# Kernel optimization log

Hardware: AMD Instinct MI355X
Metric: run time of the kernel (lower is better)

## Reference

```python
import jax, jax.numpy as jnp
import numpy as np

N = 40000
E = 640000
D_IN = 128
HID = 128


def _sage_conv(x_src, x_dst, edge_index, W_l, b_l, W_r):
    """PyG SAGEConv with mean aggregation.
    out = lin_l(mean_{j in N(i)} x_src[j]) + lin_r(x_dst[i])
    (lin_l carries the bias; lin_r has bias=False in PyG.)
    """
    src, dst = edge_index[0], edge_index[1]
    n = x_dst.shape[0]
    # gather neighbor (source) features, scatter-sum to targets
    msg_sum = jax.ops.segment_sum(x_src[src], dst, num_segments=n)  # [N, d]
    deg = jax.ops.segment_sum(jnp.ones((src.shape[0],), x_src.dtype), dst,
                              num_segments=n)  # [N]
    agg = msg_sum / jnp.maximum(deg, 1.0)[:, None]  # mean over in-neighbors
    return agg @ W_l + b_l + x_dst @ W_r


def setup_inputs() -> dict:
    key = jax.random.key(0)
    ks = jax.random.split(key, 8)
    s_in = 1.0 / np.sqrt(D_IN)
    s_h = 1.0 / np.sqrt(HID)
    return {
        "x": jax.random.normal(ks[0], (N, D_IN), jnp.float32),
        "edge_index": jax.random.randint(ks[1], (2, E), 0, N, jnp.int64)
                      if jax.config.jax_enable_x64 else
                      jax.random.randint(ks[1], (2, E), 0, N, jnp.int32),
        "W1_l": jax.random.normal(ks[2], (D_IN, HID), jnp.float32) * s_in,
        "b1": jax.random.normal(ks[3], (HID,), jnp.float32) * s_in,
        "W1_r": jax.random.normal(ks[4], (D_IN, HID), jnp.float32) * s_in,
        "W2_l": jax.random.normal(ks[5], (HID, HID), jnp.float32) * s_h,
        "b2": jax.random.normal(ks[6], (HID,), jnp.float32) * s_h,
        "W2_r": jax.random.normal(ks[7], (HID, HID), jnp.float32) * s_h,
    }


def reference(x, edge_index, W1_l, b1, W1_r, W2_l, b2, W2_r):
    h = _sage_conv(x, x, edge_index, W1_l, b1, W1_r)
    h = jax.nn.relu(h)
    out = _sage_conv(h, h, edge_index, W2_l, b2, W2_r)
    return out
```

## Files before the change

### kernel.cpp

```cpp
#include <hip/hip_runtime.h>
#include <hip/hip_bf16.h>

#define NN 40000
#define NE 640000
#define DD 128
#define SLOT 128

typedef unsigned short u16;
typedef unsigned int u32;
typedef __attribute__((ext_vector_type(8))) short short8v;
typedef __attribute__((ext_vector_type(4))) float f32x4;

__device__ __forceinline__ u16 f2b(float f) {
  __hip_bfloat16 h = __float2bfloat16(f);
  return *reinterpret_cast<u16*>(&h);
}

#define TOB_N (NN * DD / 4)
#define WCVT_N 65536
__global__ void setup_kernel(const float* __restrict__ x,
                             const float* __restrict__ W1l, const float* __restrict__ W1r,
                             const float* __restrict__ W2l, const float* __restrict__ W2r,
                             u16* __restrict__ xb, u16* __restrict__ wt1,
                             u16* __restrict__ wt2, int* __restrict__ cnt,
                             u16* __restrict__ hb) {
  int i = blockIdx.x * 256 + threadIdx.x;
  if (i < TOB_N) {
    float4 v = *(const float4*)(x + (size_t)i * 4);
    ushort4 o;
    o.x = f2b(v.x); o.y = f2b(v.y); o.z = f2b(v.z); o.w = f2b(v.w);
    *(ushort4*)(xb + (size_t)i * 4) = o;
  } else if (i < TOB_N + WCVT_N) {
    int j = i - TOB_N;
    int layer = j >> 15;
    int jj = j & 32767;
    int n = jj >> 8, k = jj & 255;
    const float* W = layer ? ((k < 128) ? W2l : W2r) : ((k < 128) ? W1l : W1r);
    u16* Wt = layer ? wt2 : wt1;
    Wt[jj] = f2b(W[(size_t)(k & 127) * 128 + n]);
  } else if (i < TOB_N + WCVT_N + NN) {
    cnt[i - TOB_N - WCVT_N] = 0;
  } else if (i < TOB_N + WCVT_N + NN + 128) {
    int j = i - TOB_N - WCVT_N - NN;
    u32* p = (j < 64) ? ((u32*)(xb + (size_t)NN * DD) + j)
                      : ((u32*)(hb + (size_t)NN * DD) + (j - 64));
    *p = 0u;
  }
}

__global__ void fill2_kernel(const int* __restrict__ src, const int* __restrict__ dst,
                             int* __restrict__ cnt, int* __restrict__ csr) {
  int e = blockIdx.x * 256 + threadIdx.x;
  if (e < NE) {
    int d = dst[e];
    int p = atomicAdd(&cnt[d], 1);
    if (p < SLOT) __builtin_nontemporal_store(src[e], &csr[(size_t)d * SLOT + p]);
  }
}

template <int OUT_BF16, int RELU>
__global__ __launch_bounds__(256) void fused_kernel(
    const u16* __restrict__ feat, const int* __restrict__ cnt,
    const int* __restrict__ csr, const u16* __restrict__ Wt,
    const float* __restrict__ bias, void* __restrict__ outp) {
  __shared__ u16 As[2][16][128];
  const int t = threadIdx.x;
  const int w = t >> 6;
  const int lane = t & 63;
  const int li = lane & 15;
  const int eo = lane >> 4;
  const int tile = blockIdx.x * 16;
  const int node0 = tile + w * 4;

  {
    const int j = w * 4 + eo;
    const uint4 s = *(const uint4*)(feat + (size_t)(tile + j) * DD + li * 8);
    *(uint4*)((char*)&As[1][j][0] + ((li * 16) ^ ((j & 7) << 4))) = s;
  }

  int n[4];
  float inv[4];
#pragma unroll
  for (int s = 0; s < 4; ++s) {
    const int d = cnt[node0 + s];
    n[s] = (d < SLOT) ? d : SLOT;
    inv[s] = 1.0f / (float)(d > 1 ? d : 1);
  }
  int nmax = max(max(n[0], n[1]), max(n[2], n[3]));

  float acc[4][8];
#pragma unroll
  for (int s = 0; s < 4; ++s)
#pragma unroll
    for (int j = 0; j < 8; ++j) acc[s][j] = 0.f;

  const int* crow0 = csr + (size_t)node0 * SLOT;
  for (int it = eo; it < nmax; it += 4) {
    int srcn[4];
#pragma unroll
    for (int s = 0; s < 4; ++s)
      srcn[s] = (it < n[s]) ? crow0[s * SLOT + it] : NN;
    uint4 v[4];
#pragma unroll
    for (int s = 0; s < 4; ++s)
      v[s] = *(const uint4*)(feat + (size_t)srcn[s] * DD + li * 8);
#pragma unroll
    for (int s = 0; s < 4; ++s) {
      acc[s][0] += __uint_as_float(v[s].x << 16);
      acc[s][1] += __uint_as_float(v[s].x & 0xffff0000u);
      acc[s][2] += __uint_as_float(v[s].y << 16);
      acc[s][3] += __uint_as_float(v[s].y & 0xffff0000u);
      acc[s][4] += __uint_as_float(v[s].z << 16);
      acc[s][5] += __uint_as_float(v[s].z & 0xffff0000u);
      acc[s][6] += __uint_as_float(v[s].w << 16);
      acc[s][7] += __uint_as_float(v[s].w & 0xffff0000u);
    }
  }
#pragma unroll
  for (int s = 0; s < 4; ++s)
#pragma unroll
    for (int j = 0; j < 8; ++j) {
      acc[s][j] += __shfl_xor(acc[s][j], 16, 64);
      acc[s][j] += __shfl_xor(acc[s][j], 32, 64);
    }
  if (eo == 0) {
#pragma unroll
    for (int s = 0; s < 4; ++s) {
      u16 r8[8];
#pragma unroll
      for (int j = 0; j < 8; ++j) r8[j] = f2b(acc[s][j] * inv[s]);
      uint4 o;
      o.x = (u32)r8[0] | ((u32)r8[1] << 16);
      o.y = (u32)r8[2] | ((u32)r8[3] << 16);
      o.z = (u32)r8[4] | ((u32)r8[5] << 16);
      o.w = (u32)r8[6] | ((u32)r8[7] << 16);
      const int j = w * 4 + s;
      *(uint4*)((char*)&As[0][j][0] + ((li * 16) ^ ((j & 7) << 4))) = o;
    }
  }
  __syncthreads();

  const int r = li;
  const int g = eo;
  f32x4 acc2[2];
  acc2[0] = (f32x4){0.f, 0.f, 0.f, 0.f};
  acc2[1] = (f32x4){0.f, 0.f, 0.f, 0.f};
#pragma unroll
  for (int ks = 0; ks < 8; ++ks) {
    const int sel = ks >> 2;
    const int c0 = (ks & 3) * 32 + g * 8;
    const short8v afr =
        *(const short8v*)((const char*)&As[sel][r][0] + ((c0 * 2) ^ ((r & 7) << 4)));
#pragma unroll
    for (int ntl = 0; ntl < 2; ++ntl) {
      const int col = (w * 2 + ntl) * 16 + r;
      const short8v bfr = *(const short8v*)(Wt + (size_t)col * 256 + ks * 32 + g * 8);
      acc2[ntl] = __builtin_amdgcn_mfma_f32_16x16x32_bf16(afr, bfr, acc2[ntl], 0, 0, 0);
    }
  }
#pragma unroll
  for (int ntl = 0; ntl < 2; ++ntl) {
    const int col = (w * 2 + ntl) * 16 + r;
    const float bv = bias[col];
#pragma unroll
    for (int reg = 0; reg < 4; ++reg) {
      const int row = tile + g * 4 + reg;
      float o = acc2[ntl][reg] + bv;
      if (RELU) o = fmaxf(o, 0.f);
      if (OUT_BF16)
        ((u16*)outp)[(size_t)row * DD + col] = f2b(o);
      else
        ((float*)outp)[(size_t)row * DD + col] = o;
    }
  }
}

extern "C" void kernel_launch(void* const* d_in, const int* in_sizes, int n_in,
                              void* d_out, int out_size, void* d_ws, size_t ws_size,
                              hipStream_t stream) {
  const float* x = (const float*)d_in[0];
  const int* ei = (const int*)d_in[1];
  const int* srcv = ei;
  const int* dstv = ei + NE;
  const float* W1l = (const float*)d_in[2];
  const float* b1 = (const float*)d_in[3];
  const float* W1r = (const float*)d_in[4];
  const float* W2l = (const float*)d_in[5];
  const float* b2 = (const float*)d_in[6];
  const float* W2r = (const float*)d_in[7];
  float* out = (float*)d_out;

  char* ws = (char*)d_ws;
  int* cnt = (int*)(ws + 0);
  int* csr = (int*)(ws + 160256);
  u16* xb = (u16*)(ws + 20640256);
  u16* hb = (u16*)(ws + 30880512);
  u16* wt1 = (u16*)(ws + 41120768);
  u16* wt2 = (u16*)(ws + 41186304);

  const int nbS = (TOB_N + WCVT_N + NN + 128 + 255) / 256;
  const int nbE = NE / 256;

  setup_kernel<<<nbS, 256, 0, stream>>>(x, W1l, W1r, W2l, W2r, xb, wt1, wt2, cnt, hb);
  fill2_kernel<<<nbE, 256, 0, stream>>>(srcv, dstv, cnt, csr);
  fused_kernel<1, 1><<<NN / 16, 256, 0, stream>>>(xb, cnt, csr, wt1, b1, (void*)hb);
  fused_kernel<0, 0><<<NN / 16, 256, 0, stream>>>(hb, cnt, csr, wt2, b2, (void*)out);
}
```

Measured before the change: 144.0 us.

## Chunk feature tables by column and split aggregation from the matmul

```diff
diff --git a/kernel.cpp b/kernel.cpp
--- a/kernel.cpp
+++ b/kernel.cpp
@@ -4,10 +4,14 @@
 #define NN 40000
 #define NE 640000
 #define DD 128
-#define SLOT 128
+#define SLOT 64
+#define CH 4
+#define CW 32
+#define NT (NN / 16)
 
 typedef unsigned short u16;
 typedef unsigned int u32;
+typedef unsigned long long u64;
 typedef __attribute__((ext_vector_type(8))) short short8v;
 typedef __attribute__((ext_vector_type(4))) float f32x4;
 
@@ -16,67 +20,72 @@
   return *reinterpret_cast<u16*>(&h);
 }
 
-#define TOB_N (NN * DD / 4)
+#define XROW ((NN + 1) * CW)
+#define AROW (NN * CW)
+
+#define XCVT_N (CH * NN * 4)
 #define WCVT_N 65536
 __global__ void setup_kernel(const float* __restrict__ x,
                              const float* __restrict__ W1l, const float* __restrict__ W1r,
                              const float* __restrict__ W2l, const float* __restrict__ W2r,
-                             u16* __restrict__ xb, u16* __restrict__ wt1,
+                             u16* __restrict__ xbT, u16* __restrict__ wt1,
                              u16* __restrict__ wt2, int* __restrict__ cnt,
-                             u16* __restrict__ hb) {
+                             u16* __restrict__ hbT) {
   int i = blockIdx.x * 256 + threadIdx.x;
-  if (i < TOB_N) {
-    float4 v = *(const float4*)(x + (size_t)i * 4);
-    ushort4 o;
-    o.x = f2b(v.x); o.y = f2b(v.y); o.z = f2b(v.z); o.w = f2b(v.w);
-    *(ushort4*)(xb + (size_t)i * 4) = o;
-  } else if (i < TOB_N + WCVT_N) {
-    int j = i - TOB_N;
+  if (i < XCVT_N) {
+    int j = i & 3;
+    int node = (i >> 2) % NN;
+    int c = (i >> 2) / NN;
+    const float* src = x + (size_t)node * DD + c * CW + j * 8;
+    float4 a = *(const float4*)src;
+    float4 b = *(const float4*)(src + 4);
+    u16 r[8] = {f2b(a.x), f2b(a.y), f2b(a.z), f2b(a.w),
+                f2b(b.x), f2b(b.y), f2b(b.z), f2b(b.w)};
+    *(uint4*)(xbT + (size_t)c * XROW + (size_t)node * CW + j * 8) = *(uint4*)r;
+  } else if (i < XCVT_N + WCVT_N) {
+    int j = i - XCVT_N;
     int layer = j >> 15;
     int jj = j & 32767;
     int n = jj >> 8, k = jj & 255;
     const float* W = layer ? ((k < 128) ? W2l : W2r) : ((k < 128) ? W1l : W1r);
     u16* Wt = layer ? wt2 : wt1;
     Wt[jj] = f2b(W[(size_t)(k & 127) * 128 + n]);
-  } else if (i < TOB_N + WCVT_N + NN) {
-    cnt[i - TOB_N - WCVT_N] = 0;
-  } else if (i < TOB_N + WCVT_N + NN + 128) {
-    int j = i - TOB_N - WCVT_N - NN;
-    u32* p = (j < 64) ? ((u32*)(xb + (size_t)NN * DD) + j)
-                      : ((u32*)(hb + (size_t)NN * DD) + (j - 64));
-    *p = 0u;
+  } else if (i < XCVT_N + WCVT_N + NN) {
+    cnt[i - XCVT_N - WCVT_N] = 0;
+  } else if (i < XCVT_N + WCVT_N + NN + 2 * CH * CW) {
+    int j = i - XCVT_N - WCVT_N - NN;
+    int tbl = j >> 7;
+    int jj = j & 127;
+    int c = jj >> 5, e = jj & 31;
+    u16* p = (tbl ? hbT : xbT) + (size_t)c * XROW + (size_t)NN * CW + e;
+    *p = 0;
   }
 }
 
 __global__ void fill2_kernel(const int* __restrict__ src, const int* __restrict__ dst,
-                             int* __restrict__ cnt, int* __restrict__ csr) {
+                             int* __restrict__ cnt, u16* __restrict__ csr) {
   int e = blockIdx.x * 256 + threadIdx.x;
   if (e < NE) {
     int d = dst[e];
     int p = atomicAdd(&cnt[d], 1);
-    if (p < SLOT) __builtin_nontemporal_store(src[e], &csr[(size_t)d * SLOT + p]);
-  }
-}
-
-template <int OUT_BF16, int RELU>
-__global__ __launch_bounds__(256) void fused_kernel(
-    const u16* __restrict__ feat, const int* __restrict__ cnt,
-    const int* __restrict__ csr, const u16* __restrict__ Wt,
-    const float* __restrict__ bias, void* __restrict__ outp) {
-  __shared__ u16 As[2][16][128];
+    if (p < SLOT)
+      __builtin_nontemporal_store((u16)src[e], &csr[(size_t)d * SLOT + p]);
+  }
+}
+
+__global__ __launch_bounds__(256) void agg_kernel(
+    const u16* __restrict__ featT, const int* __restrict__ cnt,
+    const u16* __restrict__ csr, u16* __restrict__ aggT) {
+  const int bid = blockIdx.x;
+  const int c = bid / NT;
+  const int tile = (bid % NT) * 16;
   const int t = threadIdx.x;
   const int w = t >> 6;
   const int lane = t & 63;
-  const int li = lane & 15;
-  const int eo = lane >> 4;
-  const int tile = blockIdx.x * 16;
+  const int li = lane & 7;
+  const int slot = lane >> 3;
   const int node0 = tile + w * 4;
-
-  {
-    const int j = w * 4 + eo;
-    const uint4 s = *(const uint4*)(feat + (size_t)(tile + j) * DD + li * 8);
-    *(uint4*)((char*)&As[1][j][0] + ((li * 16) ^ ((j & 7) << 4))) = s;
-  }
+  const u16* xc = featT + (size_t)c * XROW;
 
   int n[4];
   float inv[4];
@@ -86,89 +95,97 @@
     n[s] = (d < SLOT) ? d : SLOT;
     inv[s] = 1.0f / (float)(d > 1 ? d : 1);
   }
-  int nmax = max(max(n[0], n[1]), max(n[2], n[3]));
-
-  float acc[4][8];
+  const int nmax = max(max(n[0], n[1]), max(n[2], n[3]));
+
+  float acc[4][4];
 #pragma unroll
   for (int s = 0; s < 4; ++s)
 #pragma unroll
-    for (int j = 0; j < 8; ++j) acc[s][j] = 0.f;
-
-  const int* crow0 = csr + (size_t)node0 * SLOT;
-  for (int it = eo; it < nmax; it += 4) {
+    for (int j = 0; j < 4; ++j) acc[s][j] = 0.f;
+
+  const u16* crow = csr + (size_t)node0 * SLOT;
+  for (int it = slot; it < nmax; it += 8) {
     int srcn[4];
 #pragma unroll
     for (int s = 0; s < 4; ++s)
-      srcn[s] = (it < n[s]) ? crow0[s * SLOT + it] : NN;
-    uint4 v[4];
+      srcn[s] = (it < n[s]) ? (int)crow[s * SLOT + it] : NN;
+    uint2 v[4];
 #pragma unroll
     for (int s = 0; s < 4; ++s)
-      v[s] = *(const uint4*)(feat + (size_t)srcn[s] * DD + li * 8);
+      v[s] = *(const uint2*)(xc + (size_t)srcn[s] * CW + li * 4);
 #pragma unroll
     for (int s = 0; s < 4; ++s) {
       acc[s][0] += __uint_as_float(v[s].x << 16);
       acc[s][1] += __uint_as_float(v[s].x & 0xffff0000u);
       acc[s][2] += __uint_as_float(v[s].y << 16);
       acc[s][3] += __uint_as_float(v[s].y & 0xffff0000u);
-      acc[s][4] += __uint_as_float(v[s].z << 16);
-      acc[s][5] += __uint_as_float(v[s].z & 0xffff0000u);
-      acc[s][6] += __uint_as_float(v[s].w << 16);
-      acc[s][7] += __uint_as_float(v[s].w & 0xffff0000u);
     }
   }
 #pragma unroll
   for (int s = 0; s < 4; ++s)
 #pragma unroll
-    for (int j = 0; j < 8; ++j) {
+    for (int j = 0; j < 4; ++j) {
+      acc[s][j] += __shfl_xor(acc[s][j], 8, 64);
       acc[s][j] += __shfl_xor(acc[s][j], 16, 64);
       acc[s][j] += __shfl_xor(acc[s][j], 32, 64);
     }
-  if (eo == 0) {
+  if (slot == 0) {
 #pragma unroll
     for (int s = 0; s < 4; ++s) {
-      u16 r8[8];
-#pragma unroll
-      for (int j = 0; j < 8; ++j) r8[j] = f2b(acc[s][j] * inv[s]);
-      uint4 o;
-      o.x = (u32)r8[0] | ((u32)r8[1] << 16);
-      o.y = (u32)r8[2] | ((u32)r8[3] << 16);
-      o.z = (u32)r8[4] | ((u32)r8[5] << 16);
-      o.w = (u32)r8[6] | ((u32)r8[7] << 16);
-      const int j = w * 4 + s;
-      *(uint4*)((char*)&As[0][j][0] + ((li * 16) ^ ((j & 7) << 4))) = o;
-    }
-  }
-  __syncthreads();
-
-  const int r = li;
-  const int g = eo;
-  f32x4 acc2[2];
-  acc2[0] = (f32x4){0.f, 0.f, 0.f, 0.f};
-  acc2[1] = (f32x4){0.f, 0.f, 0.f, 0.f};
+      u16 r4[4] = {f2b(acc[s][0] * inv[s]), f2b(acc[s][1] * inv[s]),
+                   f2b(acc[s][2] * inv[s]), f2b(acc[s][3] * inv[s])};
+      u64 packed;
+      __builtin_memcpy(&packed, r4, 8);
+      __builtin_nontemporal_store(
+          packed,
+          (u64*)(aggT + (size_t)c * AROW + (size_t)(node0 + s) * CW + li * 4));
+    }
+  }
+}
+
+template <int OUT_CHUNKED, int RELU>
+__global__ __launch_bounds__(256) void mm_kernel(
+    const u16* __restrict__ aggT, const u16* __restrict__ selfT,
+    const u16* __restrict__ Wt, const float* __restrict__ bias,
+    void* __restrict__ outp) {
+  const int t = threadIdx.x;
+  const int w = t >> 6;
+  const int lane = t & 63;
+  const int r = lane & 15;
+  const int g = lane >> 4;
+  const int m0 = blockIdx.x * 64 + w * 16;
+
+  f32x4 acc[8];
+#pragma unroll
+  for (int i = 0; i < 8; ++i) acc[i] = (f32x4){0.f, 0.f, 0.f, 0.f};
+
 #pragma unroll
   for (int ks = 0; ks < 8; ++ks) {
-    const int sel = ks >> 2;
-    const int c0 = (ks & 3) * 32 + g * 8;
-    const short8v afr =
-        *(const short8v*)((const char*)&As[sel][r][0] + ((c0 * 2) ^ ((r & 7) << 4)));
-#pragma unroll
-    for (int ntl = 0; ntl < 2; ++ntl) {
-      const int col = (w * 2 + ntl) * 16 + r;
-      const short8v bfr = *(const short8v*)(Wt + (size_t)col * 256 + ks * 32 + g * 8);
-      acc2[ntl] = __builtin_amdgcn_mfma_f32_16x16x32_bf16(afr, bfr, acc2[ntl], 0, 0, 0);
-    }
-  }
-#pragma unroll
-  for (int ntl = 0; ntl < 2; ++ntl) {
-    const int col = (w * 2 + ntl) * 16 + r;
+    const u16* ap = (ks < 4)
+        ? aggT + (size_t)ks * AROW + (size_t)(m0 + r) * CW + g * 8
+        : selfT + (size_t)(ks - 4) * XROW + (size_t)(m0 + r) * CW + g * 8;
+    const short8v afr = *(const short8v*)ap;
+#pragma unroll
+    for (int nt = 0; nt < 8; ++nt) {
+      const short8v bfr =
+          *(const short8v*)(Wt + (size_t)(nt * 16 + r) * 256 + ks * 32 + g * 8);
+      acc[nt] = __builtin_amdgcn_mfma_f32_16x16x32_bf16(afr, bfr, acc[nt], 0, 0, 0);
+    }
+  }
+
+  const int crow0 = m0 + g * 4;
+#pragma unroll
+  for (int nt = 0; nt < 8; ++nt) {
+    const int col = nt * 16 + r;
     const float bv = bias[col];
 #pragma unroll
     for (int reg = 0; reg < 4; ++reg) {
-      const int row = tile + g * 4 + reg;
-      float o = acc2[ntl][reg] + bv;
+      const int row = crow0 + reg;
+      float o = acc[nt][reg] + bv;
       if (RELU) o = fmaxf(o, 0.f);
-      if (OUT_BF16)
-        ((u16*)outp)[(size_t)row * DD + col] = f2b(o);
+      if (OUT_CHUNKED)
+        ((u16*)outp)[(size_t)(col >> 5) * XROW + (size_t)row * CW + (col & 31)] =
+            f2b(o);
       else
         ((float*)outp)[(size_t)row * DD + col] = o;
     }
@@ -192,17 +209,21 @@
 
   char* ws = (char*)d_ws;
   int* cnt = (int*)(ws + 0);
-  int* csr = (int*)(ws + 160256);
-  u16* xb = (u16*)(ws + 20640256);
-  u16* hb = (u16*)(ws + 30880512);
-  u16* wt1 = (u16*)(ws + 41120768);
-  u16* wt2 = (u16*)(ws + 41186304);
-
-  const int nbS = (TOB_N + WCVT_N + NN + 128 + 255) / 256;
+  u16* csr = (u16*)(ws + 160256);
+  u16* aggT = (u16*)(ws + 5280256);
+  u16* xbT = (u16*)(ws + 15520256);
+  u16* hbT = (u16*)(ws + 25760512);
+  u16* wt1 = (u16*)(ws + 36000768);
+  u16* wt2 = (u16*)(ws + 36066304);
+
+  const int nbS = (XCVT_N + WCVT_N + NN + 2 * CH * CW + 255) / 256;
   const int nbE = NE / 256;
 
-  setup_kernel<<<nbS, 256, 0, stream>>>(x, W1l, W1r, W2l, W2r, xb, wt1, wt2, cnt, hb);
+  setup_kernel<<<nbS, 256, 0, stream>>>(x, W1l, W1r, W2l, W2r, xbT, wt1, wt2, cnt, hbT);
   fill2_kernel<<<nbE, 256, 0, stream>>>(srcv, dstv, cnt, csr);
-  fused_kernel<1, 1><<<NN / 16, 256, 0, stream>>>(xb, cnt, csr, wt1, b1, (void*)hb);
-  fused_kernel<0, 0><<<NN / 16, 256, 0, stream>>>(hb, cnt, csr, wt2, b2, (void*)out);
-}
+
+  agg_kernel<<<CH * NT, 256, 0, stream>>>(xbT, cnt, csr, aggT);
+  mm_kernel<1, 1><<<NN / 64, 256, 0, stream>>>(aggT, xbT, wt1, b1, (void*)hbT);
+  agg_kernel<<<CH * NT, 256, 0, stream>>>(hbT, cnt, csr, aggT);
+  mm_kernel<0, 0><<<NN / 64, 256, 0, stream>>>(aggT, hbT, wt2, b2, (void*)out);
+}
```

Result: slower. 177.9 us (+23.6%).
